# Kernel optimization log

Measured on AMD Instinct MI355X. Metric: run time of the kernel, lower is better.

Reference implementation:

```python
import jax, jax.numpy as jnp
import numpy as np

K = 7            # kernel_size (odd)
R = K // 2       # neighborhood radius
NH = 16          # num_heads


def _starts(L):
    """NATTEN (dilation=1) window start and rpb start per query index."""
    i = jnp.arange(L)
    win = jnp.clip(i - R, 0, L - K)  # key-window start (window clamped inside image)
    pb = jnp.where(i < R, 2 * R - i, jnp.where(i + R >= L, L - 1 - i, R))
    return win, pb


def setup_inputs() -> dict:
    key = jax.random.key(0)
    ks = jax.random.split(key, 12)
    B, H, W, C = 2, 128, 128, 512
    std = 0.02
    return {
        "q": jax.random.normal(ks[0], (B, H, W, C), jnp.float32),
        "k": jax.random.normal(ks[1], (B, H, W, C), jnp.float32),
        "v": jax.random.normal(ks[2], (B, H, W, C), jnp.float32),
        "wq": jax.random.normal(ks[3], (C, C), jnp.float32) * std,
        "bq": jnp.zeros((C,), jnp.float32),
        "wk": jax.random.normal(ks[4], (C, C), jnp.float32) * std,
        "bk": jnp.zeros((C,), jnp.float32),
        "wv": jax.random.normal(ks[5], (C, C), jnp.float32) * std,
        "bv": jnp.zeros((C,), jnp.float32),
        "rpb": jax.random.normal(ks[6], (NH, 2 * K - 1, 2 * K - 1), jnp.float32) * std,
        "wo": jax.random.normal(ks[7], (C, C), jnp.float32) * std,
        "bo": jnp.zeros((C,), jnp.float32),
    }


def reference(q, k, v, wq, bq, wk, bk, wv, bv, rpb, wo, bo):
    B, H, W, C = q.shape
    hd = C // NH
    scale = hd ** -0.5

    def proj(x, w, b):
        y = x @ w.T + b  # torch nn.Linear
        return y.reshape(B, H, W, NH, hd).transpose(0, 3, 1, 2, 4)  # [B,nh,H,W,hd]

    qh = proj(q, wq, bq) * scale
    kh = proj(k, wk, bk)
    vh = proj(v, wv, bv)

    # H,W (128) >= window_size (7): torch padding branch is dead and omitted.
    sh, ph = _starts(H)
    sw, pw = _starts(W)

    # natten2dqkrpb: per-offset shifted-row/col gathers; never materialize
    # the dense [B,nh,H,W,k*k,hd] unfold.
    logits = []
    for a in range(K):
        kh_a = kh[:, :, sh + a]          # [B,nh,H,W,hd]
        rpb_a = rpb[:, ph + a]           # [nh,H,2K-1]
        for b in range(K):
            k_ab = kh_a[:, :, :, sw + b]             # [B,nh,H,W,hd]
            bias = rpb_a[:, :, pw + b]               # [nh,H,W]
            logits.append(jnp.einsum("bnhwd,bnhwd->bnhw", qh, k_ab) + bias[None])
    attn = jax.nn.softmax(jnp.stack(logits, axis=-1), axis=-1)  # [B,nh,H,W,K*K]

    # natten2dav
    x = jnp.zeros_like(qh)
    for a in range(K):
        vh_a = vh[:, :, sh + a]
        for b in range(K):
            v_ab = vh_a[:, :, :, sw + b]
            x = x + attn[..., a * K + b, None] * v_ab

    x = x.transpose(0, 2, 3, 1, 4).reshape(B, H, W, C)
    return x @ wo.T + bo
```

## Files before the change

kernel.cpp:

```cpp
#include <hip/hip_runtime.h>
#include <hip/hip_bf16.h>

typedef __attribute__((ext_vector_type(8))) short          s16x8;
typedef __attribute__((ext_vector_type(8))) unsigned short u16x8;
typedef __attribute__((ext_vector_type(4))) float          f4;

__device__ __forceinline__ float bf2f(unsigned short u) {
    union { unsigned int i; float f; } x; x.i = ((unsigned int)u) << 16; return x.f;
}
__device__ __forceinline__ unsigned short f2bf(float f) {
    __hip_bfloat16 h = __float2bfloat16(f);
    return *reinterpret_cast<unsigned short*>(&h);
}
__device__ __forceinline__ void gload_lds16(const void* g, void* l) {
    __builtin_amdgcn_global_load_lds(
        (const __attribute__((address_space(1))) unsigned int*)g,
        (__attribute__((address_space(3))) unsigned int*)l, 16, 0, 0);
}

__global__ __launch_bounds__(256) void cvt_w4(const float* __restrict__ a,
                                              const float* __restrict__ b,
                                              const float* __restrict__ c,
                                              const float* __restrict__ d,
                                              unsigned short* __restrict__ o) {
    const int i   = (blockIdx.x * 256 + threadIdx.x) * 8;
    const int seg = i >> 18;
    const int off = i & 262143;
    const float* s = (seg == 0) ? a : (seg == 1) ? b : (seg == 2) ? c : d;
    f4 x0 = *(const f4*)(s + off);
    f4 x1 = *(const f4*)(s + off + 4);
    unsigned short t[8];
    t[0] = f2bf(x0[0]); t[1] = f2bf(x0[1]); t[2] = f2bf(x0[2]); t[3] = f2bf(x0[3]);
    t[4] = f2bf(x1[0]); t[5] = f2bf(x1[1]); t[6] = f2bf(x1[2]); t[7] = f2bf(x1[3]);
    *(u16x8*)(o + i) = *(u16x8*)t;
}

template <bool AF32, bool OF32>
__global__ __launch_bounds__(256, 2) void gemm_fn(const void* __restrict__ Ap,
                                                  const unsigned short* __restrict__ Wb,
                                                  const float* __restrict__ bias,
                                                  void* __restrict__ Outp,
                                                  float scale) {
    constexpr int KD = 512, BK = 32, NT = KD / BK;
    constexpr int ASZ = AF32 ? 64 * BK * 4 : 64 * BK * 2;
    constexpr int WSZ = 512 * BK * 2;
    constexpr int STRIDE = ASZ + WSZ;
    extern __shared__ unsigned char lds[];

    const int tid  = threadIdx.x;
    const int lane = tid & 63;
    const int w    = tid >> 6;
    const size_t m0 = (size_t)blockIdx.x * 64;

    const float*          Af = (const float*)Ap;
    const unsigned short* Ab = (const unsigned short*)Ap;

    const int fr = lane & 15;
    const int j4 = lane >> 4;

    f4 acc[4][8];
#pragma unroll
    for (int i = 0; i < 4; ++i)
#pragma unroll
        for (int j = 0; j < 8; ++j) acc[i][j] = (f4)(0.0f);

    auto stage = [&](int t, int buf) {
        const int kt = t * BK;
        unsigned char* base = lds + buf * STRIDE;
        if constexpr (AF32) {
#pragma unroll
            for (int i = 0; i < 2; ++i) {
                const int f = i * 256 + tid;
                const int row = f >> 3, p = f & 7;
                const int s = p ^ (row & 7);
                gload_lds16(Af + (m0 + row) * KD + kt + s * 4, base + f * 16);
            }
        } else {
            const int f = tid;
            const int l = f ^ ((f >> 3) & 7);
            gload_lds16(Ab + (m0 + (l >> 2)) * KD + kt + (l & 3) * 8, base + f * 16);
        }
#pragma unroll
        for (int i = 0; i < 8; ++i) {
            const int f = i * 256 + tid;
            const int l = f ^ ((f >> 3) & 7);
            gload_lds16(Wb + (size_t)(l >> 2) * KD + kt + (l & 3) * 8,
                        base + ASZ + f * 16);
        }
    };

    stage(0, 0);
    stage(1, 1);

    for (int t = 0; t < NT; ++t) {
        const int buf = t & 1;
        unsigned char* base = lds + buf * STRIDE;
        if (t + 1 < NT) {
            if constexpr (AF32) asm volatile("s_waitcnt vmcnt(10)" ::: "memory");
            else                asm volatile("s_waitcnt vmcnt(9)"  ::: "memory");
        } else {
            asm volatile("s_waitcnt vmcnt(0)" ::: "memory");
        }
        __builtin_amdgcn_s_barrier();
        __builtin_amdgcn_sched_barrier(0);

        s16x8 af[4];
#pragma unroll
        for (int mi = 0; mi < 4; ++mi) {
            const int row = mi * 16 + fr;
            if constexpr (AF32) {
                const int r7 = row & 7;
                const int s0 = j4 * 2;
                f4 x0 = *(const f4*)(base + row * 128 + ((s0 ^ r7) << 4));
                f4 x1 = *(const f4*)(base + row * 128 + (((s0 + 1) ^ r7) << 4));
                unsigned short u[8];
                u[0] = f2bf(x0[0]); u[1] = f2bf(x0[1]); u[2] = f2bf(x0[2]); u[3] = f2bf(x0[3]);
                u[4] = f2bf(x1[0]); u[5] = f2bf(x1[1]); u[6] = f2bf(x1[2]); u[7] = f2bf(x1[3]);
                af[mi] = *(s16x8*)u;
            } else {
                const int L = (row << 2) | j4;
                const int P = L ^ ((L >> 3) & 7);
                af[mi] = *(const s16x8*)(base + (P << 4));
            }
        }
#pragma unroll
        for (int ni = 0; ni < 8; ++ni) {
            const int nrow = w * 128 + ni * 16 + fr;
            const int L = (nrow << 2) | j4;
            const int P = L ^ ((L >> 3) & 7);
            const s16x8 bf = *(const s16x8*)(base + ASZ + (P << 4));
#pragma unroll
            for (int mi = 0; mi < 4; ++mi)
                acc[mi][ni] = __builtin_amdgcn_mfma_f32_16x16x32_bf16(
                    af[mi], bf, acc[mi][ni], 0, 0, 0);
        }

        __builtin_amdgcn_sched_barrier(0);
        __builtin_amdgcn_s_barrier();
        __builtin_amdgcn_sched_barrier(0);
        if (t + 2 < NT) stage(t + 2, buf);
    }

    const int rq = (lane >> 4) << 2;
#pragma unroll
    for (int ni = 0; ni < 8; ++ni) {
        const int   col = w * 128 + ni * 16 + fr;
        const float bv  = bias[col];
#pragma unroll
        for (int mi = 0; mi < 4; ++mi) {
            const size_t rbase = m0 + mi * 16 + rq;
#pragma unroll
            for (int r = 0; r < 4; ++r) {
                const float val = (acc[mi][ni][r] + bv) * scale;
                if constexpr (OF32)
                    ((float*)Outp)[(rbase + r) * KD + col] = val;
                else
                    ((unsigned short*)Outp)[(rbase + r) * KD + col] = f2bf(val);
            }
        }
    }
}

__global__ __launch_bounds__(256) void natt(const unsigned short* __restrict__ qh,
                                            const unsigned short* __restrict__ kh,
                                            const unsigned short* __restrict__ vh,
                                            const float* __restrict__ rpb,
                                            unsigned short* __restrict__ xout) {
    constexpr int LDK = 40;
    __shared__ unsigned short KV[484][LDK];
    __shared__ float Rs[169];

    const int tid = threadIdx.x;
    const int h   = blockIdx.z & 15;
    const int b   = blockIdx.z >> 4;
    const int x0  = blockIdx.x * 16;
    const int y0  = blockIdx.y * 16;
    const int ux0 = min(max(x0 - 3, 0), 106);
    const int uy0 = min(max(y0 - 3, 0), 106);
    const int tx  = tid & 15;
    const int ty  = tid >> 4;
    const int x   = x0 + tx;
    const int y   = y0 + ty;

    if (tid < 169) Rs[tid] = rpb[h * 169 + tid];

    const long imgbase = (long)b * 128 * 128;

#pragma unroll 2
    for (int kk = tid; kk < 484; kk += 256) {
        const int ky = uy0 + kk / 22;
        const int kx = ux0 + kk % 22;
        const unsigned short* src = kh + (imgbase + ky * 128 + kx) * 512 + h * 32;
#pragma unroll
        for (int j = 0; j < 4; ++j)
            *(u16x8*)&KV[kk][j * 8] = *(const u16x8*)(src + j * 8);
    }

    const long pix = imgbase + y * 128 + x;
    const unsigned short* qp = qh + pix * 512 + h * 32;
    float qv[32];
#pragma unroll
    for (int j = 0; j < 4; ++j) {
        u16x8 v = *(const u16x8*)(qp + j * 8);
#pragma unroll
        for (int e = 0; e < 8; ++e) qv[j * 8 + e] = bf2f(v[e]);
    }

    const int myy = min(max(y - 3, 0), 121) - uy0;
    const int myx = min(max(x - 3, 0), 121) - ux0;
    const int pbY = (y < 3) ? (6 - y) : ((y >= 125) ? (127 - y) : 3);
    const int pbX = (x < 3) ? (6 - x) : ((x >= 125) ? (127 - x) : 3);

    __syncthreads();

    float logit[49];
#pragma unroll
    for (int a = 0; a < 7; ++a) {
        const int rowk = (myy + a) * 22 + myx;
#pragma unroll
        for (int c = 0; c < 7; ++c) {
            const unsigned short* kp = &KV[rowk + c][0];
            float s = 0.f;
#pragma unroll
            for (int j = 0; j < 4; ++j) {
                u16x8 v = *(const u16x8*)(kp + j * 8);
#pragma unroll
                for (int e = 0; e < 8; ++e) s = fmaf(qv[j * 8 + e], bf2f(v[e]), s);
            }
            logit[a * 7 + c] = s + Rs[(pbY + a) * 13 + pbX + c];
        }
    }

    float m = logit[0];
#pragma unroll
    for (int i = 1; i < 49; ++i) m = fmaxf(m, logit[i]);
    float sum = 0.f;
#pragma unroll
    for (int i = 0; i < 49; ++i) {
        float p = exp2f((logit[i] - m) * 1.4426950408889634f);
        logit[i] = p;
        sum += p;
    }
    const float rinv = 1.f / sum;
#pragma unroll
    for (int i = 0; i < 49; ++i) logit[i] *= rinv;

    __syncthreads();

#pragma unroll 2
    for (int kk = tid; kk < 484; kk += 256) {
        const int ky = uy0 + kk / 22;
        const int kx = ux0 + kk % 22;
        const unsigned short* src = vh + (imgbase + ky * 128 + kx) * 512 + h * 32;
#pragma unroll
        for (int j = 0; j < 4; ++j)
            *(u16x8*)&KV[kk][j * 8] = *(const u16x8*)(src + j * 8);
    }
    __syncthreads();

    float acc[32];
#pragma unroll
    for (int d = 0; d < 32; ++d) acc[d] = 0.f;
#pragma unroll
    for (int a = 0; a < 7; ++a) {
        const int rowk = (myy + a) * 22 + myx;
#pragma unroll
        for (int c = 0; c < 7; ++c) {
            const unsigned short* vp = &KV[rowk + c][0];
            const float wgt = logit[a * 7 + c];
#pragma unroll
            for (int j = 0; j < 4; ++j) {
                u16x8 v = *(const u16x8*)(vp + j * 8);
#pragma unroll
                for (int e = 0; e < 8; ++e)
                    acc[j * 8 + e] = fmaf(wgt, bf2f(v[e]), acc[j * 8 + e]);
            }
        }
    }

    unsigned short* op = xout + pix * 512 + h * 32;
#pragma unroll
    for (int j = 0; j < 4; ++j) {
        unsigned short t[8];
#pragma unroll
        for (int e = 0; e < 8; ++e) t[e] = f2bf(acc[j * 8 + e]);
        *(u16x8*)(op + j * 8) = *(u16x8*)t;
    }
}

extern "C" void kernel_launch(void* const* d_in, const int* in_sizes, int n_in,
                              void* d_out, int out_size, void* d_ws, size_t ws_size,
                              hipStream_t stream) {
    const float* q   = (const float*)d_in[0];
    const float* k   = (const float*)d_in[1];
    const float* v   = (const float*)d_in[2];
    const float* wq  = (const float*)d_in[3];
    const float* bq  = (const float*)d_in[4];
    const float* wk  = (const float*)d_in[5];
    const float* bk  = (const float*)d_in[6];
    const float* wv  = (const float*)d_in[7];
    const float* bv  = (const float*)d_in[8];
    const float* rpb = (const float*)d_in[9];
    const float* wo  = (const float*)d_in[10];
    const float* bo  = (const float*)d_in[11];

    const long P = 2l * 128 * 128;
    unsigned short* qh = (unsigned short*)d_ws;
    unsigned short* kh = qh + P * 512;
    unsigned short* vh = kh + P * 512;
    unsigned short* xb = vh + P * 512;
    unsigned short* Wb = xb + P * 512;

    const float scale = 0.17677669529663687f;

    const size_t smemF = 2 * (64 * 32 * 4 + 512 * 32 * 2);
    const size_t smemB = 2 * (64 * 32 * 2 + 512 * 32 * 2);

    cvt_w4<<<512, 256, 0, stream>>>(wq, wk, wv, wo, Wb);

    gemm_fn<true, false><<<512, 256, smemF, stream>>>(q, Wb,          bq, qh, scale);
    gemm_fn<true, false><<<512, 256, smemF, stream>>>(k, Wb + 262144, bk, kh, 1.0f);
    gemm_fn<true, false><<<512, 256, smemF, stream>>>(v, Wb + 524288, bv, vh, 1.0f);

    natt<<<dim3(8, 8, 32), 256, 0, stream>>>(qh, kh, vh, rpb, xb);

    gemm_fn<false, true><<<512, 256, smemB, stream>>>(xb, Wb + 786432, bo, (float*)d_out, 1.0f);
}
```

Measured before the change: 264.4 us.

## Switch intermediates to fp16, use fdot2 in attention, merge QKV projection launches

Replaces the bf16 storage and MFMA with fp16, converting through packed round-toward-zero conversions. The attention logits now use v_dot2 fp16 instructions with two accumulators, which cuts the unpack-and-FMA work. The three Q/K/V projection GEMMs become a single launch with a 3-wide grid y dimension, and the natt launch bounds ask for 4 blocks per CU. fp16 has a narrower range than bf16, and rtz rounding may raise error, which could be a risk if activations are large.

```diff
diff --git a/kernel.cpp b/kernel.cpp
--- a/kernel.cpp
+++ b/kernel.cpp
@@ -1,16 +1,17 @@
 #include <hip/hip_runtime.h>
 #include <hip/hip_bf16.h>
 
-typedef __attribute__((ext_vector_type(8))) short          s16x8;
+typedef __attribute__((ext_vector_type(8))) _Float16       h8;
+typedef __attribute__((ext_vector_type(2))) _Float16       h2;
 typedef __attribute__((ext_vector_type(8))) unsigned short u16x8;
 typedef __attribute__((ext_vector_type(4))) float          f4;
-
-__device__ __forceinline__ float bf2f(unsigned short u) {
-    union { unsigned int i; float f; } x; x.i = ((unsigned int)u) << 16; return x.f;
-}
-__device__ __forceinline__ unsigned short f2bf(float f) {
-    __hip_bfloat16 h = __float2bfloat16(f);
-    return *reinterpret_cast<unsigned short*>(&h);
+typedef __attribute__((ext_vector_type(4))) unsigned int   u32x4;
+typedef __attribute__((ext_vector_type(2))) unsigned int   u32x2;
+
+__device__ __forceinline__ h2 bch2(unsigned int w) { return __builtin_bit_cast(h2, w); }
+__device__ __forceinline__ unsigned int pkrtz(float a, float b) {
+    auto r = __builtin_amdgcn_cvt_pkrtz(a, b);
+    return __builtin_bit_cast(unsigned int, r);
 }
 __device__ __forceinline__ void gload_lds16(const void* g, void* l) {
     __builtin_amdgcn_global_load_lds(
@@ -29,23 +30,25 @@
     const float* s = (seg == 0) ? a : (seg == 1) ? b : (seg == 2) ? c : d;
     f4 x0 = *(const f4*)(s + off);
     f4 x1 = *(const f4*)(s + off + 4);
-    unsigned short t[8];
-    t[0] = f2bf(x0[0]); t[1] = f2bf(x0[1]); t[2] = f2bf(x0[2]); t[3] = f2bf(x0[3]);
-    t[4] = f2bf(x1[0]); t[5] = f2bf(x1[1]); t[6] = f2bf(x1[2]); t[7] = f2bf(x1[3]);
-    *(u16x8*)(o + i) = *(u16x8*)t;
+    u32x4 t;
+    t[0] = pkrtz(x0[0], x0[1]);
+    t[1] = pkrtz(x0[2], x0[3]);
+    t[2] = pkrtz(x1[0], x1[1]);
+    t[3] = pkrtz(x1[2], x1[3]);
+    *(u32x4*)(o + i) = t;
 }
 
 template <bool AF32, bool OF32>
-__global__ __launch_bounds__(256, 2) void gemm_fn(const void* __restrict__ Ap,
-                                                  const unsigned short* __restrict__ Wb,
-                                                  const float* __restrict__ bias,
-                                                  void* __restrict__ Outp,
-                                                  float scale) {
+__device__ __forceinline__ void gemm_body(const void* __restrict__ Ap,
+                                          const unsigned short* __restrict__ Wb,
+                                          const float* __restrict__ bias,
+                                          void* __restrict__ Outp,
+                                          float scale,
+                                          unsigned char* lds) {
     constexpr int KD = 512, BK = 32, NT = KD / BK;
     constexpr int ASZ = AF32 ? 64 * BK * 4 : 64 * BK * 2;
     constexpr int WSZ = 512 * BK * 2;
     constexpr int STRIDE = ASZ + WSZ;
-    extern __shared__ unsigned char lds[];
 
     const int tid  = threadIdx.x;
     const int lane = tid & 63;
@@ -104,7 +107,7 @@
         __builtin_amdgcn_s_barrier();
         __builtin_amdgcn_sched_barrier(0);
 
-        s16x8 af[4];
+        h8 af[4];
 #pragma unroll
         for (int mi = 0; mi < 4; ++mi) {
             const int row = mi * 16 + fr;
@@ -113,14 +116,16 @@
                 const int s0 = j4 * 2;
                 f4 x0 = *(const f4*)(base + row * 128 + ((s0 ^ r7) << 4));
                 f4 x1 = *(const f4*)(base + row * 128 + (((s0 + 1) ^ r7) << 4));
-                unsigned short u[8];
-                u[0] = f2bf(x0[0]); u[1] = f2bf(x0[1]); u[2] = f2bf(x0[2]); u[3] = f2bf(x0[3]);
-                u[4] = f2bf(x1[0]); u[5] = f2bf(x1[1]); u[6] = f2bf(x1[2]); u[7] = f2bf(x1[3]);
-                af[mi] = *(s16x8*)u;
+                u32x4 t4;
+                t4[0] = pkrtz(x0[0], x0[1]);
+                t4[1] = pkrtz(x0[2], x0[3]);
+                t4[2] = pkrtz(x1[0], x1[1]);
+                t4[3] = pkrtz(x1[2], x1[3]);
+                af[mi] = __builtin_bit_cast(h8, t4);
             } else {
                 const int L = (row << 2) | j4;
                 const int P = L ^ ((L >> 3) & 7);
-                af[mi] = *(const s16x8*)(base + (P << 4));
+                af[mi] = *(const h8*)(base + (P << 4));
             }
         }
 #pragma unroll
@@ -128,10 +133,10 @@
             const int nrow = w * 128 + ni * 16 + fr;
             const int L = (nrow << 2) | j4;
             const int P = L ^ ((L >> 3) & 7);
-            const s16x8 bf = *(const s16x8*)(base + ASZ + (P << 4));
+            const h8 bf = *(const h8*)(base + ASZ + (P << 4));
 #pragma unroll
             for (int mi = 0; mi < 4; ++mi)
-                acc[mi][ni] = __builtin_amdgcn_mfma_f32_16x16x32_bf16(
+                acc[mi][ni] = __builtin_amdgcn_mfma_f32_16x16x32_f16(
                     af[mi], bf, acc[mi][ni], 0, 0, 0);
         }
 
@@ -152,20 +157,51 @@
 #pragma unroll
             for (int r = 0; r < 4; ++r) {
                 const float val = (acc[mi][ni][r] + bv) * scale;
-                if constexpr (OF32)
+                if constexpr (OF32) {
                     ((float*)Outp)[(rbase + r) * KD + col] = val;
-                else
-                    ((unsigned short*)Outp)[(rbase + r) * KD + col] = f2bf(val);
-            }
-        }
-    }
-}
-
-__global__ __launch_bounds__(256) void natt(const unsigned short* __restrict__ qh,
-                                            const unsigned short* __restrict__ kh,
-                                            const unsigned short* __restrict__ vh,
-                                            const float* __restrict__ rpb,
-                                            unsigned short* __restrict__ xout) {
+                } else {
+                    const _Float16 hv = (_Float16)val;
+                    ((unsigned short*)Outp)[(rbase + r) * KD + col] =
+                        __builtin_bit_cast(unsigned short, hv);
+                }
+            }
+        }
+    }
+}
+
+__global__ __launch_bounds__(256, 2) void gemm_proj3(const float* __restrict__ q,
+                                                     const float* __restrict__ k,
+                                                     const float* __restrict__ v,
+                                                     const unsigned short* __restrict__ Wb,
+                                                     const float* __restrict__ bq,
+                                                     const float* __restrict__ bk,
+                                                     const float* __restrict__ bv,
+                                                     unsigned short* __restrict__ qh,
+                                                     unsigned short* __restrict__ kh,
+                                                     unsigned short* __restrict__ vh,
+                                                     float scale) {
+    extern __shared__ unsigned char lds[];
+    const int by = blockIdx.y;
+    const float*          A  = (by == 0) ? q  : (by == 1) ? k  : v;
+    const float*          bi = (by == 0) ? bq : (by == 1) ? bk : bv;
+    unsigned short*       O  = (by == 0) ? qh : (by == 1) ? kh : vh;
+    gemm_body<true, false>(A, Wb + (size_t)by * 262144, bi, O,
+                           (by == 0) ? scale : 1.0f, lds);
+}
+
+__global__ __launch_bounds__(256, 2) void gemm_outk(const unsigned short* __restrict__ Xb,
+                                                    const unsigned short* __restrict__ Wb,
+                                                    const float* __restrict__ bias,
+                                                    float* __restrict__ Out) {
+    extern __shared__ unsigned char lds[];
+    gemm_body<false, true>(Xb, Wb, bias, Out, 1.0f, lds);
+}
+
+__global__ __launch_bounds__(256, 4) void natt(const unsigned short* __restrict__ qh,
+                                               const unsigned short* __restrict__ kh,
+                                               const unsigned short* __restrict__ vh,
+                                               const float* __restrict__ rpb,
+                                               unsigned short* __restrict__ xout) {
     constexpr int LDK = 40;
     __shared__ unsigned short KV[484][LDK];
     __shared__ float Rs[169];
@@ -198,12 +234,15 @@
 
     const long pix = imgbase + y * 128 + x;
     const unsigned short* qp = qh + pix * 512 + h * 32;
-    float qv[32];
-#pragma unroll
-    for (int j = 0; j < 4; ++j) {
-        u16x8 v = *(const u16x8*)(qp + j * 8);
-#pragma unroll
-        for (int e = 0; e < 8; ++e) qv[j * 8 + e] = bf2f(v[e]);
+    h2 qv[16];
+    {
+        const u32x4* q32 = (const u32x4*)qp;
+#pragma unroll
+        for (int j = 0; j < 4; ++j) {
+            const u32x4 wv = q32[j];
+#pragma unroll
+            for (int e = 0; e < 4; ++e) qv[j * 4 + e] = bch2(wv[e]);
+        }
     }
 
     const int myy = min(max(y - 3, 0), 121) - uy0;
@@ -219,15 +258,17 @@
         const int rowk = (myy + a) * 22 + myx;
 #pragma unroll
         for (int c = 0; c < 7; ++c) {
-            const unsigned short* kp = &KV[rowk + c][0];
-            float s = 0.f;
+            const u32x4* kp = (const u32x4*)&KV[rowk + c][0];
+            float s0 = 0.f, s1 = 0.f;
 #pragma unroll
             for (int j = 0; j < 4; ++j) {
-                u16x8 v = *(const u16x8*)(kp + j * 8);
-#pragma unroll
-                for (int e = 0; e < 8; ++e) s = fmaf(qv[j * 8 + e], bf2f(v[e]), s);
-            }
-            logit[a * 7 + c] = s + Rs[(pbY + a) * 13 + pbX + c];
+                const u32x4 wv = kp[j];
+                s0 = __builtin_amdgcn_fdot2(qv[4 * j + 0], bch2(wv[0]), s0, false);
+                s1 = __builtin_amdgcn_fdot2(qv[4 * j + 1], bch2(wv[1]), s1, false);
+                s0 = __builtin_amdgcn_fdot2(qv[4 * j + 2], bch2(wv[2]), s0, false);
+                s1 = __builtin_amdgcn_fdot2(qv[4 * j + 3], bch2(wv[3]), s1, false);
+            }
+            logit[a * 7 + c] = s0 + s1 + Rs[(pbY + a) * 13 + pbX + c];
         }
     }
 
@@ -266,14 +307,17 @@
         const int rowk = (myy + a) * 22 + myx;
 #pragma unroll
         for (int c = 0; c < 7; ++c) {
-            const unsigned short* vp = &KV[rowk + c][0];
+            const u32x4* vp = (const u32x4*)&KV[rowk + c][0];
             const float wgt = logit[a * 7 + c];
 #pragma unroll
             for (int j = 0; j < 4; ++j) {
-                u16x8 v = *(const u16x8*)(vp + j * 8);
-#pragma unroll
-                for (int e = 0; e < 8; ++e)
-                    acc[j * 8 + e] = fmaf(wgt, bf2f(v[e]), acc[j * 8 + e]);
+                const u32x4 wv = vp[j];
+#pragma unroll
+                for (int e = 0; e < 4; ++e) {
+                    const h2 hv = bch2(wv[e]);
+                    acc[8 * j + 2 * e]     = fmaf((float)hv[0], wgt, acc[8 * j + 2 * e]);
+                    acc[8 * j + 2 * e + 1] = fmaf((float)hv[1], wgt, acc[8 * j + 2 * e + 1]);
+                }
             }
         }
     }
@@ -281,10 +325,14 @@
     unsigned short* op = xout + pix * 512 + h * 32;
 #pragma unroll
     for (int j = 0; j < 4; ++j) {
-        unsigned short t[8];
-#pragma unroll
-        for (int e = 0; e < 8; ++e) t[e] = f2bf(acc[j * 8 + e]);
-        *(u16x8*)(op + j * 8) = *(u16x8*)t;
+        u32x2 p;
+        p[0] = pkrtz(acc[8 * j + 0], acc[8 * j + 1]);
+        p[1] = pkrtz(acc[8 * j + 2], acc[8 * j + 3]);
+        u32x2 p2;
+        p2[0] = pkrtz(acc[8 * j + 4], acc[8 * j + 5]);
+        p2[1] = pkrtz(acc[8 * j + 6], acc[8 * j + 7]);
+        *(u32x2*)(op + j * 8)     = p;
+        *(u32x2*)(op + j * 8 + 4) = p2;
     }
 }
 
@@ -312,17 +360,15 @@
     unsigned short* Wb = xb + P * 512;
 
     const float scale = 0.17677669529663687f;
-
     const size_t smemF = 2 * (64 * 32 * 4 + 512 * 32 * 2);
     const size_t smemB = 2 * (64 * 32 * 2 + 512 * 32 * 2);
 
     cvt_w4<<<512, 256, 0, stream>>>(wq, wk, wv, wo, Wb);
 
-    gemm_fn<true, false><<<512, 256, smemF, stream>>>(q, Wb,          bq, qh, scale);
-    gemm_fn<true, false><<<512, 256, smemF, stream>>>(k, Wb + 262144, bk, kh, 1.0f);
-    gemm_fn<true, false><<<512, 256, smemF, stream>>>(v, Wb + 524288, bv, vh, 1.0f);
+    gemm_proj3<<<dim3(512, 3, 1), 256, smemF, stream>>>(
+        q, k, v, Wb, bq, bk, bv, qh, kh, vh, scale);
 
     natt<<<dim3(8, 8, 32), 256, 0, stream>>>(qh, kh, vh, rpb, xb);
 
-    gemm_fn<false, true><<<512, 256, smemB, stream>>>(xb, Wb + 786432, bo, (float*)d_out, 1.0f);
-}
+    gemm_outk<<<512, 256, smemB, stream>>>(xb, Wb + 786432, bo, (float*)d_out);
+}
```

After: 222.1 us (median of 3 runs). 1.19x faster.
